# Kernel tuning notes

Measured on AMD Instinct MI355X. Metric: run time of the kernel, lower is better.

## Reference

```python
import jax, jax.numpy as jnp
import numpy as np

N_USER, N_REST, D, E, Q = 200000, 50000, 64, 2000000, 500000


def setup_inputs() -> dict:
    key = jax.random.key(0)
    ks = jax.random.split(key, 16)
    s = 0.05
    return {
        "x_user": jax.random.normal(ks[0], (N_USER, D), jnp.float32),
        "x_rest": jax.random.normal(ks[1], (N_REST, D), jnp.float32),
        "Wl": jax.random.normal(ks[2], (3, 2, D, D), jnp.float32) * s,
        "Wr": jax.random.normal(ks[3], (3, 2, D, D), jnp.float32) * s,
        "bl": jnp.zeros((3, 2, D), jnp.float32),
        "dW1": jax.random.normal(ks[4], (D, 2 * D), jnp.float32) * s,
        "db1": jnp.zeros((D,), jnp.float32),
        "dW2": jax.random.normal(ks[5], (D, D), jnp.float32) * s,
        "db2": jnp.zeros((D,), jnp.float32),
        "dW3": jax.random.normal(ks[6], (1, D), jnp.float32) * s,
        "db3": jnp.zeros((1,), jnp.float32),
        "ur_src": jax.random.randint(ks[7], (E,), 0, N_USER, jnp.int32),
        "ur_dst": jax.random.randint(ks[8], (E,), 0, N_REST, jnp.int32),
        "ru_src": jax.random.randint(ks[9], (E,), 0, N_REST, jnp.int32),
        "ru_dst": jax.random.randint(ks[10], (E,), 0, N_USER, jnp.int32),
        "el_row": jax.random.randint(ks[11], (Q,), 0, N_USER, jnp.int32),
        "el_col": jax.random.randint(ks[12], (Q,), 0, N_REST, jnp.int32),
    }


def _sage(h_src, h_dst, src, dst, W_l, b_l, W_r):
    # PyG SAGEConv: lin_l(mean_{j in N(i)} x_j) + lin_r(x_i); bias on lin_l only.
    n_dst = h_dst.shape[0]
    agg = jax.ops.segment_sum(h_src[src], dst, num_segments=n_dst)  # [n_dst, D]
    cnt = jax.ops.segment_sum(jnp.ones_like(dst, dtype=h_src.dtype), dst, num_segments=n_dst)
    mean = agg / jnp.maximum(cnt, 1)[:, None]
    return mean @ W_l.T + b_l + h_dst @ W_r.T


def reference(x_user, x_rest, Wl, Wr, bl, dW1, db1, dW2, db2, dW3, db3,
              ur_src, ur_dst, ru_src, ru_dst, el_row, el_col):
    hu, hr = x_user, x_rest
    for l in range(3):
        # edge type 0: user -> restaurant ('rates'); edge type 1: reverse
        zr = _sage(hu, hr, ur_src, ur_dst, Wl[l, 0], bl[l, 0], Wr[l, 0])
        zu = _sage(hr, hu, ru_src, ru_dst, Wl[l, 1], bl[l, 1], Wr[l, 1])
        if l < 2:
            zr, zu = jax.nn.relu(zr), jax.nn.relu(zu)
        hu, hr = zu, zr
    # EdgeDecoder
    z = jnp.concatenate([hu[el_row], hr[el_col]], axis=-1)  # [Q, 2D]
    z = jax.nn.relu(z @ dW1.T + db1)
    z = jax.nn.relu(z @ dW2.T + db2)
    z = z @ dW3.T + db3
    return z.reshape(-1)
```

## Files before the change

### kernel.cpp

```cpp
#include <hip/hip_runtime.h>

#define NU 200000
#define NR 50000
#define DD 64
#define NE 2000000
#define NQ 500000
#define NBR 196
#define NBU 782

#define NBS 98
#define BKT_CAP 24576
#define LW_U 11
#define LW_R 9
#define PB_E 4096
#define NPBB 489

__global__ __launch_bounds__(256)
void binpass_kernel(const int* __restrict__ ru_src, const int* __restrict__ ru_dst,
                    const int* __restrict__ ur_src, const int* __restrict__ ur_dst,
                    int* __restrict__ bcur, int2* __restrict__ pairs) {
    __shared__ int2 stg[PB_E];
    __shared__ unsigned char gstg[PB_E];
    __shared__ int hist[256];
    __shared__ int sca[256], scb[256];
    __shared__ int gpos[128];
    int side = (blockIdx.x >= NPBB) ? 1 : 0;
    int blk = side ? (blockIdx.x - NPBB) : blockIdx.x;
    const int* src = side ? ur_src : ru_src;
    const int* dst = side ? ur_dst : ru_dst;
    int lw = side ? LW_R : LW_U;
    int* bc = bcur + side * NBS;
    int2* region = pairs + (size_t)side * NBS * BKT_CAP;
    int tid = threadIdx.x;
    hist[tid] = 0;
    __syncthreads();
    int base = blk * PB_E;
    int myg[16]; int myrank[16]; int2 myp[16];
#pragma unroll
    for (int i = 0; i < 16; i++) {
        int e = base + i * 256 + tid;
        if (e < NE) {
            int d = dst[e];
            int g = d >> lw;
            myg[i] = g;
            myp[i] = make_int2(src[e], d);
            myrank[i] = atomicAdd(&hist[g], 1);
        } else myg[i] = -1;
    }
    __syncthreads();
    int h = hist[tid];
    sca[tid] = h;
    __syncthreads();
    int* cur = sca; int* alt = scb;
    for (int off = 1; off < 256; off <<= 1) {
        int x = cur[tid];
        if (tid >= off) x += cur[tid - off];
        alt[tid] = x;
        __syncthreads();
        int* tmp = cur; cur = alt; alt = tmp;
    }
    alt[tid] = cur[tid] - h;
    if (tid < NBS && h > 0) gpos[tid] = atomicAdd(&bc[tid], h);
    __syncthreads();
    int* basep = alt;
#pragma unroll
    for (int i = 0; i < 16; i++) {
        if (myg[i] >= 0) {
            int p = basep[myg[i]] + myrank[i];
            stg[p] = myp[i];
            gstg[p] = (unsigned char)myg[i];
        }
    }
    __syncthreads();
    int tot = cur[255];
    for (int i = tid; i < tot; i += 256) {
        int g = gstg[i];
        int o = g * BKT_CAP + gpos[g] + (i - basep[g]);
        region[o] = stg[i];
    }
}

__global__ void bbase_kernel(const int* __restrict__ bcur, int* __restrict__ bbase,
                             int* __restrict__ rs_u, int* __restrict__ rs_r) {
    __shared__ int a[128], b[128];
    int sidx = blockIdx.x;
    const int* bc = bcur + sidx * NBS;
    int* bb = bbase + sidx * NBS;
    int tid = threadIdx.x;
    a[tid] = (tid < NBS) ? bc[tid] : 0;
    __syncthreads();
    int* cur = a; int* alt = b;
    for (int off = 1; off < 128; off <<= 1) {
        int t = cur[tid];
        if (tid >= off) t += cur[tid - off];
        alt[tid] = t;
        __syncthreads();
        int* tmp = cur; cur = alt; alt = tmp;
    }
    if (tid < NBS) bb[tid] = (tid == 0) ? 0 : cur[tid - 1];
    if (tid == 0) { if (sidx == 0) rs_u[NU] = NE; else rs_r[NR] = NE; }
}

__global__ __launch_bounds__(256)
void fillpass_kernel(const int2* __restrict__ pairs, const int* __restrict__ bcur,
                     const int* __restrict__ bbase,
                     int* __restrict__ rs_u, int* __restrict__ rs_r,
                     int* __restrict__ csr_u, int* __restrict__ csr_r) {
    __shared__ int win[BKT_CAP];
    __shared__ int lcnt[2048];
    __shared__ int lofs[2048];
    __shared__ int tsc[256], tsc2[256];
    int side = (blockIdx.x >= NBS) ? 1 : 0;
    int bkt = side ? (blockIdx.x - NBS) : blockIdx.x;
    const int2* reg = pairs + ((size_t)side * NBS + bkt) * BKT_CAP;
    int* rs = side ? rs_r : rs_u;
    int* csr = side ? csr_r : csr_u;
    int W = side ? 512 : 2048;
    int lw = side ? LW_R : LW_U;
    int n = side ? NR : NU;
    int d0 = bkt << lw;
    int tot = bcur[side * NBS + bkt];
    int base = bbase[side * NBS + bkt];
    int tid = threadIdx.x;
    for (int i = tid; i < W; i += 256) lcnt[i] = 0;
    __syncthreads();
    for (int i = tid; i < tot; i += 256) {
        int2 p = reg[i];
        atomicAdd(&lcnt[p.y - d0], 1);
    }
    __syncthreads();
    int per = W >> 8;
    int b0 = tid * per;
    int run = 0;
    for (int i = 0; i < per; i++) { int v = lcnt[b0 + i]; lofs[b0 + i] = run; run += v; }
    tsc[tid] = run;
    __syncthreads();
    int* cur = tsc; int* alt = tsc2;
    for (int off = 1; off < 256; off <<= 1) {
        int x = cur[tid];
        if (tid >= off) x += cur[tid - off];
        alt[tid] = x;
        __syncthreads();
        int* tmp = cur; cur = alt; alt = tmp;
    }
    int texcl = cur[tid] - run;
    for (int i = 0; i < per; i++) lofs[b0 + i] += texcl;
    __syncthreads();
    int wn = min(W, n - d0);
    for (int i = tid; i < wn; i += 256) rs[d0 + i] = base + lofs[i];
    __syncthreads();
    for (int i = tid; i < tot; i += 256) {
        int2 p = reg[i];
        int slot = atomicAdd(&lofs[p.y - d0], 1);
        win[slot] = p.x;
    }
    __syncthreads();
    for (int i = tid; i < tot; i += 256) csr[base + i] = win[i];
}

__global__ __launch_bounds__(256)
void gather2_kernel(const float* __restrict__ hu, const int* __restrict__ csr_r,
                    const int* __restrict__ rs_r, float* __restrict__ mean_r,
                    const float* __restrict__ hr, const int* __restrict__ csr_u,
                    const int* __restrict__ rs_u, float* __restrict__ mean_u) {
    int lane = threadIdx.x & 63;
    int wave = blockIdx.x * 4 + (threadIdx.x >> 6);
    const float* h; const int* csr; const int* rs; float* mean; int r;
    if (wave < NR) { h = hu; csr = csr_r; rs = rs_r; mean = mean_r; r = wave; }
    else if (wave < NR + NU) { h = hr; csr = csr_u; rs = rs_u; mean = mean_u; r = wave - NR; }
    else return;
    int s = rs[r], e = rs[r + 1];
    float a0 = 0.f, a1 = 0.f, a2 = 0.f, a3 = 0.f;
    for (int j = s; j < e; j += 64) {
        int rem = e - j;
        int nch = rem < 64 ? rem : 64;
        int li = lane < nch ? lane : nch - 1;
        int idx = csr[j + li];
        for (int kk = 0; kk < nch; kk += 4) {
            int i0 = __shfl(idx, kk);
            int i1 = __shfl(idx, kk + 1);
            int i2 = __shfl(idx, kk + 2);
            int i3 = __shfl(idx, kk + 3);
            float v0 = h[i0 * DD + lane];
            float v1 = h[i1 * DD + lane];
            float v2 = h[i2 * DD + lane];
            float v3 = h[i3 * DD + lane];
            a0 += v0;
            a1 += (kk + 1 < nch) ? v1 : 0.f;
            a2 += (kk + 2 < nch) ? v2 : 0.f;
            a3 += (kk + 3 < nch) ? v3 : 0.f;
        }
    }
    float acc = (a0 + a1) + (a2 + a3);
    float inv = 1.0f / fmaxf((float)(e - s), 1.0f);
    mean[r * DD + lane] = acc * inv;
}

#define DOT4(A, B) ((A).x*(B).x + (A).y*(B).y + (A).z*(B).z + (A).w*(B).w)

#define SDECL(j) float sA##j = bsh[cb + (j)], sB##j = sA##j, sC##j = sA##j, sD##j = sA##j;

#define SCOL(j) { \
    const float4* wlp_ = (const float4*)(Wls + ((cb + (j)) << 6) + kc); \
    const float4* wrp_ = (const float4*)(Wrs + ((cb + (j)) << 6) + kc); \
    float4 l0_ = wlp_[0], l1_ = wlp_[1], q0_ = wrp_[0], q1_ = wrp_[1]; \
    sA##j += DOT4(mA0,l0_)+DOT4(mA1,l1_)+DOT4(xA0,q0_)+DOT4(xA1,q1_); \
    sB##j += DOT4(mB0,l0_)+DOT4(mB1,l1_)+DOT4(xB0,q0_)+DOT4(xB1,q1_); \
    sC##j += DOT4(mC0,l0_)+DOT4(mC1,l1_)+DOT4(xC0,q0_)+DOT4(xC1,q1_); \
    sD##j += DOT4(mD0,l0_)+DOT4(mD1,l1_)+DOT4(xD0,q0_)+DOT4(xD1,q1_); }

#define SRELU(j) { sA##j = fmaxf(sA##j,0.f); sB##j = fmaxf(sB##j,0.f); \
                   sC##j = fmaxf(sC##j,0.f); sD##j = fmaxf(sD##j,0.f); }

#define STORE_ROW(SR, rr) if ((rr) < n) { \
    float* o_ = out + (size_t)(rr) * DD + cb; \
    *(float4*)(o_)      = {SR##0,  SR##1,  SR##2,  SR##3}; \
    *(float4*)(o_ + 4)  = {SR##4,  SR##5,  SR##6,  SR##7}; \
    *(float4*)(o_ + 8)  = {SR##8,  SR##9,  SR##10, SR##11}; \
    *(float4*)(o_ + 12) = {SR##12, SR##13, SR##14, SR##15}; }

__device__ __forceinline__
void sage_tile(const float* __restrict__ mean, const float* __restrict__ h,
               const float* Wls, const float* Wrs, const float* bsh,
               float* __restrict__ out, int n, int do_relu, int r0, int cb) {
    int rA = min(r0, n - 1), rB = min(r0 + 64, n - 1);
    int rC = min(r0 + 128, n - 1), rD = min(r0 + 192, n - 1);
    const float *mA = mean + (size_t)rA * DD, *xA = h + (size_t)rA * DD;
    const float *mB = mean + (size_t)rB * DD, *xB = h + (size_t)rB * DD;
    const float *mC = mean + (size_t)rC * DD, *xC = h + (size_t)rC * DD;
    const float *mD = mean + (size_t)rD * DD, *xD = h + (size_t)rD * DD;
    SDECL(0)  SDECL(1)  SDECL(2)  SDECL(3)  SDECL(4)  SDECL(5)  SDECL(6)  SDECL(7)
    SDECL(8)  SDECL(9)  SDECL(10) SDECL(11) SDECL(12) SDECL(13) SDECL(14) SDECL(15)
#pragma unroll 1
    for (int kc = 0; kc < DD; kc += 8) {
        float4 mA0 = *(const float4*)(mA + kc), mA1 = *(const float4*)(mA + kc + 4);
        float4 xA0 = *(const float4*)(xA + kc), xA1 = *(const float4*)(xA + kc + 4);
        float4 mB0 = *(const float4*)(mB + kc), mB1 = *(const float4*)(mB + kc + 4);
        float4 xB0 = *(const float4*)(xB + kc), xB1 = *(const float4*)(xB + kc + 4);
        float4 mC0 = *(const float4*)(mC + kc), mC1 = *(const float4*)(mC + kc + 4);
        float4 xC0 = *(const float4*)(xC + kc), xC1 = *(const float4*)(xC + kc + 4);
        float4 mD0 = *(const float4*)(mD + kc), mD1 = *(const float4*)(mD + kc + 4);
        float4 xD0 = *(const float4*)(xD + kc), xD1 = *(const float4*)(xD + kc + 4);
        SCOL(0)  SCOL(1)  SCOL(2)  SCOL(3)  SCOL(4)  SCOL(5)  SCOL(6)  SCOL(7)
        SCOL(8)  SCOL(9)  SCOL(10) SCOL(11) SCOL(12) SCOL(13) SCOL(14) SCOL(15)
    }
    if (do_relu) {
        SRELU(0)  SRELU(1)  SRELU(2)  SRELU(3)  SRELU(4)  SRELU(5)  SRELU(6)  SRELU(7)
        SRELU(8)  SRELU(9)  SRELU(10) SRELU(11) SRELU(12) SRELU(13) SRELU(14) SRELU(15)
    }
    STORE_ROW(sA, r0)
    STORE_ROW(sB, r0 + 64)
    STORE_ROW(sC, r0 + 128)
    STORE_ROW(sD, r0 + 192)
}

__global__ __launch_bounds__(256, 2)
void sage_fused_kernel(const float* __restrict__ mean_r, const float* __restrict__ hr,
                       const float* __restrict__ mean_u, const float* __restrict__ hu,
                       const float* __restrict__ Wl2, const float* __restrict__ Wr2,
                       const float* __restrict__ bl2,
                       float* __restrict__ out_r, float* __restrict__ out_u, int do_relu) {
    __shared__ float Wls[DD * DD];
    __shared__ float Wrs[DD * DD];
    __shared__ float bsh[DD];
    int side = (blockIdx.x < NBR) ? 0 : 1;
    const float* Wl = Wl2 + side * DD * DD;
    const float* Wr = Wr2 + side * DD * DD;
    const float* bl = bl2 + side * DD;
    for (int i = threadIdx.x; i < DD * DD; i += 256) {
        Wls[i] = Wl[i];
        Wrs[i] = Wr[i];
    }
    if (threadIdx.x < DD) bsh[threadIdx.x] = bl[threadIdx.x];
    __syncthreads();
    int lane = threadIdx.x & 63;
    int cb = (threadIdx.x >> 6) * 16;
    if (side == 0) {
        int r0 = blockIdx.x * 256 + lane;
        sage_tile(mean_r, hr, Wls, Wrs, bsh, out_r, NR, do_relu, r0, cb);
    } else {
        int r0 = (blockIdx.x - NBR) * 256 + lane;
        sage_tile(mean_u, hu, Wls, Wrs, bsh, out_u, NU, do_relu, r0, cb);
    }
}

#define PCOL(j) { \
    const float4* wp_ = (const float4*)(Ws + ((cb + (j)) << 6) + kc); \
    float4 w0_ = wp_[0], w1_ = wp_[1]; \
    sA##j += DOT4(xA0,w0_)+DOT4(xA1,w1_); \
    sB##j += DOT4(xB0,w0_)+DOT4(xB1,w1_); \
    sC##j += DOT4(xC0,w0_)+DOT4(xC1,w1_); \
    sD##j += DOT4(xD0,w0_)+DOT4(xD1,w1_); }

__device__ __forceinline__
void pre_tile(const float* __restrict__ h, const float* Ws, const float* bsh,
              float* __restrict__ out, int n, int r0, int cb) {
    int rA = min(r0, n - 1), rB = min(r0 + 64, n - 1);
    int rC = min(r0 + 128, n - 1), rD = min(r0 + 192, n - 1);
    const float *xA = h + (size_t)rA * DD, *xB = h + (size_t)rB * DD;
    const float *xC = h + (size_t)rC * DD, *xD = h + (size_t)rD * DD;
    SDECL(0)  SDECL(1)  SDECL(2)  SDECL(3)  SDECL(4)  SDECL(5)  SDECL(6)  SDECL(7)
    SDECL(8)  SDECL(9)  SDECL(10) SDECL(11) SDECL(12) SDECL(13) SDECL(14) SDECL(15)
#pragma unroll 1
    for (int kc = 0; kc < DD; kc += 8) {
        float4 xA0 = *(const float4*)(xA + kc), xA1 = *(const float4*)(xA + kc + 4);
        float4 xB0 = *(const float4*)(xB + kc), xB1 = *(const float4*)(xB + kc + 4);
        float4 xC0 = *(const float4*)(xC + kc), xC1 = *(const float4*)(xC + kc + 4);
        float4 xD0 = *(const float4*)(xD + kc), xD1 = *(const float4*)(xD + kc + 4);
        PCOL(0)  PCOL(1)  PCOL(2)  PCOL(3)  PCOL(4)  PCOL(5)  PCOL(6)  PCOL(7)
        PCOL(8)  PCOL(9)  PCOL(10) PCOL(11) PCOL(12) PCOL(13) PCOL(14) PCOL(15)
    }
    STORE_ROW(sA, r0)
    STORE_ROW(sB, r0 + 64)
    STORE_ROW(sC, r0 + 128)
    STORE_ROW(sD, r0 + 192)
}

__global__ __launch_bounds__(256, 2)
void pre_fused_kernel(const float* __restrict__ hu, const float* __restrict__ hr,
                      const float* __restrict__ dW1, const float* __restrict__ db1,
                      float* __restrict__ P_u, float* __restrict__ P_r) {
    __shared__ float Ws[DD * DD];
    __shared__ float bsh[DD];
    int side = (blockIdx.x < NBU) ? 0 : 1;
    int koff = side ? DD : 0;
    for (int i = threadIdx.x; i < DD * DD; i += 256) {
        int c = i >> 6, k = i & 63;
        Ws[c * DD + k] = dW1[c * 2 * DD + koff + k];
    }
    if (threadIdx.x < DD) bsh[threadIdx.x] = side ? 0.f : db1[threadIdx.x];
    __syncthreads();
    int lane = threadIdx.x & 63;
    int cb = (threadIdx.x >> 6) * 16;
    if (side == 0) {
        int r0 = blockIdx.x * 256 + lane;
        pre_tile(hu, Ws, bsh, P_u, NU, r0, cb);
    } else {
        int r0 = (blockIdx.x - NBU) * 256 + lane;
        pre_tile(hr, Ws, bsh, P_r, NR, r0, cb);
    }
}

#define ZCOMB(Zi, i) float4 Zi; { float4 u_ = pu[i]; float4 v_ = pr[i]; \
    Zi.x = fmaxf(u_.x + v_.x, 0.f); Zi.y = fmaxf(u_.y + v_.y, 0.f); \
    Zi.z = fmaxf(u_.z + v_.z, 0.f); Zi.w = fmaxf(u_.w + v_.w, 0.f); }

__global__ __launch_bounds__(256, 2)
void decoder_kernel(const float* __restrict__ Pu, const float* __restrict__ Pr,
                    const int* __restrict__ el_row, const int* __restrict__ el_col,
                    const float* __restrict__ dW2, const float* __restrict__ db2,
                    const float* __restrict__ dW3, const float* __restrict__ db3,
                    float* __restrict__ out) {
    __shared__ float W2s[DD * DD];
    __shared__ float b2s[DD], w3s[DD];
    for (int i = threadIdx.x; i < DD * DD; i += 256) W2s[i] = dW2[i];
    if (threadIdx.x < DD) {
        b2s[threadIdx.x] = db2[threadIdx.x];
        w3s[threadIdx.x] = dW3[threadIdx.x];
    }
    __syncthreads();
    int q = blockIdx.x * 256 + threadIdx.x;
    if (q >= NQ) return;
    int row = el_row[q], col = el_col[q];
    const float4* pu = (const float4*)(Pu + (size_t)row * DD);
    const float4* pr = (const float4*)(Pr + (size_t)col * DD);
    ZCOMB(z0, 0)  ZCOMB(z1, 1)  ZCOMB(z2, 2)  ZCOMB(z3, 3)
    ZCOMB(z4, 4)  ZCOMB(z5, 5)  ZCOMB(z6, 6)  ZCOMB(z7, 7)
    ZCOMB(z8, 8)  ZCOMB(z9, 9)  ZCOMB(z10, 10) ZCOMB(z11, 11)
    ZCOMB(z12, 12) ZCOMB(z13, 13) ZCOMB(z14, 14) ZCOMB(z15, 15)
    float o = db3[0];
#pragma unroll 2
    for (int c = 0; c < DD; c++) {
        const float4* wp = (const float4*)(W2s + c * DD);
        float s = b2s[c]
            + DOT4(z0, wp[0])  + DOT4(z1, wp[1])  + DOT4(z2, wp[2])  + DOT4(z3, wp[3])
            + DOT4(z4, wp[4])  + DOT4(z5, wp[5])  + DOT4(z6, wp[6])  + DOT4(z7, wp[7])
            + DOT4(z8, wp[8])  + DOT4(z9, wp[9])  + DOT4(z10, wp[10]) + DOT4(z11, wp[11])
            + DOT4(z12, wp[12]) + DOT4(z13, wp[13]) + DOT4(z14, wp[14]) + DOT4(z15, wp[15]);
        o += fmaxf(s, 0.f) * w3s[c];
    }
    out[q] = o;
}

extern "C" void kernel_launch(void* const* d_in, const int* in_sizes, int n_in,
                              void* d_out, int out_size, void* d_ws, size_t ws_size,
                              hipStream_t stream) {
    const float* x_user = (const float*)d_in[0];
    const float* x_rest = (const float*)d_in[1];
    const float* Wl     = (const float*)d_in[2];
    const float* Wr     = (const float*)d_in[3];
    const float* bl     = (const float*)d_in[4];
    const float* dW1    = (const float*)d_in[5];
    const float* db1    = (const float*)d_in[6];
    const float* dW2    = (const float*)d_in[7];
    const float* db2    = (const float*)d_in[8];
    const float* dW3    = (const float*)d_in[9];
    const float* db3    = (const float*)d_in[10];
    const int* ur_src   = (const int*)d_in[11];
    const int* ur_dst   = (const int*)d_in[12];
    const int* ru_src   = (const int*)d_in[13];
    const int* ru_dst   = (const int*)d_in[14];
    const int* el_row   = (const int*)d_in[15];
    const int* el_col   = (const int*)d_in[16];
    float* out = (float*)d_out;

    char* w = (char*)d_ws;
    size_t off = 0;
    auto alloc = [&](size_t bytes) -> void* {
        void* p = (void*)(w + off);
        off += (bytes + 255) & ~(size_t)255;
        return p;
    };
    float* hu0    = (float*)alloc((size_t)NU * DD * 4);
    float* hu1    = (float*)alloc((size_t)NU * DD * 4);
    float* hr0    = (float*)alloc((size_t)NR * DD * 4);
    float* hr1    = (float*)alloc((size_t)NR * DD * 4);
    float* mean_u = (float*)alloc((size_t)NU * DD * 4);
    float* mean_r = (float*)alloc((size_t)NR * DD * 4);
    int* csr_u  = (int*)alloc((size_t)NE * 4);
    int* csr_r  = (int*)alloc((size_t)NE * 4);
    int* rs_u   = (int*)alloc((size_t)(NU + 1) * 4);
    int* rs_r   = (int*)alloc((size_t)(NR + 1) * 4);
    int* bcur   = (int*)alloc((size_t)2 * NBS * 4);
    int* bbase  = (int*)alloc((size_t)2 * NBS * 4);

    int2* pairs = (int2*)mean_u;

    hipMemsetAsync(bcur, 0, (size_t)2 * NBS * 4, stream);
    binpass_kernel<<<2 * NPBB, 256, 0, stream>>>(ru_src, ru_dst, ur_src, ur_dst,
                                                 bcur, pairs);
    bbase_kernel<<<2, 128, 0, stream>>>(bcur, bbase, rs_u, rs_r);
    fillpass_kernel<<<2 * NBS, 256, 0, stream>>>(pairs, bcur, bbase,
                                                 rs_u, rs_r, csr_u, csr_r);

    const float* cu = x_user;
    const float* cr = x_rest;
    float* nu_[3] = {hu0, hu1, hu0};
    float* nr_[3] = {hr0, hr1, hr0};
    const int ggrid = (NR + NU + 3) / 4;

    for (int l = 0; l < 3; l++) {
        const float* Wl2 = Wl + (size_t)l * 2 * DD * DD;
        const float* Wr2 = Wr + (size_t)l * 2 * DD * DD;
        const float* bl2 = bl + (size_t)l * 2 * DD;
        int relu = (l < 2) ? 1 : 0;
        gather2_kernel<<<ggrid, 256, 0, stream>>>(cu, csr_r, rs_r, mean_r,
                                                  cr, csr_u, rs_u, mean_u);
        sage_fused_kernel<<<NBR + NBU, 256, 0, stream>>>(mean_r, cr, mean_u, cu,
                                                         Wl2, Wr2, bl2,
                                                         nr_[l], nu_[l], relu);
        cu = nu_[l];
        cr = nr_[l];
    }
    float* P_u = hu1;
    float* P_r = hr1;
    pre_fused_kernel<<<NBU + NBR, 256, 0, stream>>>(cu, cr, dW1, db1, P_u, P_r);
    decoder_kernel<<<(NQ + 255) / 256, 256, 0, stream>>>(P_u, P_r, el_row, el_col,
                                                         dW2, db2, dW3, db3, out);
}
```

Baseline: 1.180 ms.

## Replace restaurant-side CSR gather with source-sorted LDS scatter accumulation

Restaurant-side aggregation no longer builds a CSR. Instead, edges in each 256-destination bucket are sorted by source id and packed into (src,dst) words. A 512-thread block accumulates hu rows into a 64KB shared-memory tile with LDS atomics, so consecutive blocks read hu in roughly source order for better cache locality, and per-destination counts are computed once. This drops the restaurant CSR fill pass, but only 196 blocks run the scatter step per layer, which uses LDS atomics and gives low occupancy because of the large shared tile.

```diff
diff --git a/kernel.cpp b/kernel.cpp
--- a/kernel.cpp
+++ b/kernel.cpp
@@ -8,12 +8,15 @@
 #define NBR 196
 #define NBU 782
 
-#define NBS 98
-#define BKT_CAP 24576
+#define NBS_U 98
 #define LW_U 11
-#define LW_R 9
+#define CAP_U 24576
+#define NBS_R 196
+#define LW_R 8
+#define CAP_R 12288
 #define PB_E 4096
 #define NPBB 489
+#define SBINS 391
 
 __global__ __launch_bounds__(256)
 void binpass_kernel(const int* __restrict__ ru_src, const int* __restrict__ ru_dst,
@@ -23,14 +26,16 @@
     __shared__ unsigned char gstg[PB_E];
     __shared__ int hist[256];
     __shared__ int sca[256], scb[256];
-    __shared__ int gpos[128];
+    __shared__ int gpos[256];
     int side = (blockIdx.x >= NPBB) ? 1 : 0;
     int blk = side ? (blockIdx.x - NPBB) : blockIdx.x;
     const int* src = side ? ur_src : ru_src;
     const int* dst = side ? ur_dst : ru_dst;
     int lw = side ? LW_R : LW_U;
-    int* bc = bcur + side * NBS;
-    int2* region = pairs + (size_t)side * NBS * BKT_CAP;
+    int nbs = side ? NBS_R : NBS_U;
+    int cap = side ? CAP_R : CAP_U;
+    int* bc = bcur + (side ? NBS_U : 0);
+    int2* region = pairs + (side ? (size_t)NBS_U * CAP_U : 0);
     int tid = threadIdx.x;
     hist[tid] = 0;
     __syncthreads();
@@ -60,7 +65,7 @@
         int* tmp = cur; cur = alt; alt = tmp;
     }
     alt[tid] = cur[tid] - h;
-    if (tid < NBS && h > 0) gpos[tid] = atomicAdd(&bc[tid], h);
+    if (tid < nbs && h > 0) gpos[tid] = atomicAdd(&bc[tid], h);
     __syncthreads();
     int* basep = alt;
 #pragma unroll
@@ -75,19 +80,16 @@
     int tot = cur[255];
     for (int i = tid; i < tot; i += 256) {
         int g = gstg[i];
-        int o = g * BKT_CAP + gpos[g] + (i - basep[g]);
+        int o = g * cap + gpos[g] + (i - basep[g]);
         region[o] = stg[i];
     }
 }
 
-__global__ void bbase_kernel(const int* __restrict__ bcur, int* __restrict__ bbase,
-                             int* __restrict__ rs_u, int* __restrict__ rs_r) {
+__global__ void ubase_kernel(const int* __restrict__ bcur, int* __restrict__ bbase,
+                             int* __restrict__ rs_u) {
     __shared__ int a[128], b[128];
-    int sidx = blockIdx.x;
-    const int* bc = bcur + sidx * NBS;
-    int* bb = bbase + sidx * NBS;
     int tid = threadIdx.x;
-    a[tid] = (tid < NBS) ? bc[tid] : 0;
+    a[tid] = (tid < NBS_U) ? bcur[tid] : 0;
     __syncthreads();
     int* cur = a; int* alt = b;
     for (int off = 1; off < 128; off <<= 1) {
@@ -97,42 +99,34 @@
         __syncthreads();
         int* tmp = cur; cur = alt; alt = tmp;
     }
-    if (tid < NBS) bb[tid] = (tid == 0) ? 0 : cur[tid - 1];
-    if (tid == 0) { if (sidx == 0) rs_u[NU] = NE; else rs_r[NR] = NE; }
+    if (tid < NBS_U) bbase[tid] = (tid == 0) ? 0 : cur[tid - 1];
+    if (tid == 0) rs_u[NU] = NE;
 }
 
 __global__ __launch_bounds__(256)
-void fillpass_kernel(const int2* __restrict__ pairs, const int* __restrict__ bcur,
-                     const int* __restrict__ bbase,
-                     int* __restrict__ rs_u, int* __restrict__ rs_r,
-                     int* __restrict__ csr_u, int* __restrict__ csr_r) {
-    __shared__ int win[BKT_CAP];
+void fillpassu_kernel(const int2* __restrict__ pairs, const int* __restrict__ bcur,
+                      const int* __restrict__ bbase,
+                      int* __restrict__ rs_u, int* __restrict__ csr_u) {
+    __shared__ int win[CAP_U];
     __shared__ int lcnt[2048];
     __shared__ int lofs[2048];
     __shared__ int tsc[256], tsc2[256];
-    int side = (blockIdx.x >= NBS) ? 1 : 0;
-    int bkt = side ? (blockIdx.x - NBS) : blockIdx.x;
-    const int2* reg = pairs + ((size_t)side * NBS + bkt) * BKT_CAP;
-    int* rs = side ? rs_r : rs_u;
-    int* csr = side ? csr_r : csr_u;
-    int W = side ? 512 : 2048;
-    int lw = side ? LW_R : LW_U;
-    int n = side ? NR : NU;
-    int d0 = bkt << lw;
-    int tot = bcur[side * NBS + bkt];
-    int base = bbase[side * NBS + bkt];
+    int bkt = blockIdx.x;
+    const int2* reg = pairs + (size_t)bkt * CAP_U;
+    int d0 = bkt << LW_U;
+    int tot = bcur[bkt];
+    int base = bbase[bkt];
     int tid = threadIdx.x;
-    for (int i = tid; i < W; i += 256) lcnt[i] = 0;
+    for (int i = tid; i < 2048; i += 256) lcnt[i] = 0;
     __syncthreads();
     for (int i = tid; i < tot; i += 256) {
         int2 p = reg[i];
         atomicAdd(&lcnt[p.y - d0], 1);
     }
     __syncthreads();
-    int per = W >> 8;
-    int b0 = tid * per;
+    int b0 = tid * 8;
     int run = 0;
-    for (int i = 0; i < per; i++) { int v = lcnt[b0 + i]; lofs[b0 + i] = run; run += v; }
+    for (int i = 0; i < 8; i++) { int v = lcnt[b0 + i]; lofs[b0 + i] = run; run += v; }
     tsc[tid] = run;
     __syncthreads();
     int* cur = tsc; int* alt = tsc2;
@@ -144,10 +138,10 @@
         int* tmp = cur; cur = alt; alt = tmp;
     }
     int texcl = cur[tid] - run;
-    for (int i = 0; i < per; i++) lofs[b0 + i] += texcl;
-    __syncthreads();
-    int wn = min(W, n - d0);
-    for (int i = tid; i < wn; i += 256) rs[d0 + i] = base + lofs[i];
+    for (int i = 0; i < 8; i++) lofs[b0 + i] += texcl;
+    __syncthreads();
+    int wn = min(2048, NU - d0);
+    for (int i = tid; i < wn; i += 256) rs_u[d0 + i] = base + lofs[i];
     __syncthreads();
     for (int i = tid; i < tot; i += 256) {
         int2 p = reg[i];
@@ -155,36 +149,130 @@
         win[slot] = p.x;
     }
     __syncthreads();
-    for (int i = tid; i < tot; i += 256) csr[base + i] = win[i];
+    for (int i = tid; i < tot; i += 256) csr_u[base + i] = win[i];
 }
 
 __global__ __launch_bounds__(256)
-void gather2_kernel(const float* __restrict__ hu, const int* __restrict__ csr_r,
-                    const int* __restrict__ rs_r, float* __restrict__ mean_r,
-                    const float* __restrict__ hr, const int* __restrict__ csr_u,
+void srcsort_kernel(const int2* __restrict__ pairs, const int* __restrict__ bcur,
+                    int* __restrict__ pairs2, int* __restrict__ cnt_r) {
+    __shared__ int hist[512];
+    __shared__ int cntd[256];
+    __shared__ int tsc[256], tsc2[256];
+    int bkt = blockIdx.x;
+    const int2* reg = pairs + (size_t)NBS_U * CAP_U + (size_t)bkt * CAP_R;
+    int tot = bcur[NBS_U + bkt];
+    int d0 = bkt << LW_R;
+    int tid = threadIdx.x;
+    hist[tid] = 0; hist[tid + 256] = 0; cntd[tid] = 0;
+    __syncthreads();
+    for (int i = tid; i < tot; i += 256) {
+        int2 p = reg[i];
+        atomicAdd(&hist[p.x >> 9], 1);
+        atomicAdd(&cntd[p.y - d0], 1);
+    }
+    __syncthreads();
+    int wn = min(256, NR - d0);
+    if (tid < wn) cnt_r[d0 + tid] = cntd[tid];
+    int b0 = tid * 2;
+    int h0 = hist[b0], h1 = hist[b0 + 1];
+    int run = h0 + h1;
+    tsc[tid] = run;
+    __syncthreads();
+    int* cur = tsc; int* alt = tsc2;
+    for (int off = 1; off < 256; off <<= 1) {
+        int x = cur[tid];
+        if (tid >= off) x += cur[tid - off];
+        alt[tid] = x;
+        __syncthreads();
+        int* tmp = cur; cur = alt; alt = tmp;
+    }
+    int texcl = cur[tid] - run;
+    __syncthreads();
+    hist[b0] = texcl;
+    hist[b0 + 1] = texcl + h0;
+    __syncthreads();
+    for (int i = tid; i < tot; i += 256) {
+        int2 p = reg[i];
+        int pos = atomicAdd(&hist[p.x >> 9], 1);
+        pairs2[(size_t)bkt * CAP_R + pos] = (p.x << LW_R) | (p.y - d0);
+    }
+}
+
+__global__ __launch_bounds__(512, 1)
+void rscatter_kernel(const float* __restrict__ hu, const int* __restrict__ pairs2,
+                     const int* __restrict__ bcur, const int* __restrict__ cnt_r,
+                     float* __restrict__ mean_r) {
+    __shared__ float acc[256 * DD];
+    int bkt = blockIdx.x;
+    int tot = bcur[NBS_U + bkt];
+    int d0 = bkt << LW_R;
+    const int* reg = pairs2 + (size_t)bkt * CAP_R;
+    int tid = threadIdx.x;
+    for (int i = tid; i < 256 * DD; i += 512) acc[i] = 0.f;
+    __syncthreads();
+    int lane = tid & 63;
+    int wv = tid >> 6;
+    for (int c = wv * 64; c < tot; c += 512) {
+        int n = min(64, tot - c);
+        int v = reg[c + (lane < n ? lane : n - 1)];
+        for (int k = 0; k < n; k += 8) {
+            int v0 = __shfl(v, k);
+            int v1 = __shfl(v, k + 1);
+            int v2 = __shfl(v, k + 2);
+            int v3 = __shfl(v, k + 3);
+            int v4 = __shfl(v, k + 4);
+            int v5 = __shfl(v, k + 5);
+            int v6 = __shfl(v, k + 6);
+            int v7 = __shfl(v, k + 7);
+            float x0 = hu[(size_t)(v0 >> LW_R) * DD + lane];
+            float x1 = hu[(size_t)(v1 >> LW_R) * DD + lane];
+            float x2 = hu[(size_t)(v2 >> LW_R) * DD + lane];
+            float x3 = hu[(size_t)(v3 >> LW_R) * DD + lane];
+            float x4 = hu[(size_t)(v4 >> LW_R) * DD + lane];
+            float x5 = hu[(size_t)(v5 >> LW_R) * DD + lane];
+            float x6 = hu[(size_t)(v6 >> LW_R) * DD + lane];
+            float x7 = hu[(size_t)(v7 >> LW_R) * DD + lane];
+            atomicAdd(&acc[(v0 & 255) * DD + lane], x0);
+            if (k + 1 < n) atomicAdd(&acc[(v1 & 255) * DD + lane], x1);
+            if (k + 2 < n) atomicAdd(&acc[(v2 & 255) * DD + lane], x2);
+            if (k + 3 < n) atomicAdd(&acc[(v3 & 255) * DD + lane], x3);
+            if (k + 4 < n) atomicAdd(&acc[(v4 & 255) * DD + lane], x4);
+            if (k + 5 < n) atomicAdd(&acc[(v5 & 255) * DD + lane], x5);
+            if (k + 6 < n) atomicAdd(&acc[(v6 & 255) * DD + lane], x6);
+            if (k + 7 < n) atomicAdd(&acc[(v7 & 255) * DD + lane], x7);
+        }
+    }
+    __syncthreads();
+    int wn = min(256, NR - d0);
+    for (int rr = wv; rr < wn; rr += 8) {
+        float inv = 1.0f / fmaxf((float)cnt_r[d0 + rr], 1.0f);
+        mean_r[(size_t)(d0 + rr) * DD + lane] = acc[rr * DD + lane] * inv;
+    }
+}
+
+__global__ __launch_bounds__(256)
+void gatheru_kernel(const float* __restrict__ hr, const int* __restrict__ csr_u,
                     const int* __restrict__ rs_u, float* __restrict__ mean_u) {
     int lane = threadIdx.x & 63;
     int wave = blockIdx.x * 4 + (threadIdx.x >> 6);
-    const float* h; const int* csr; const int* rs; float* mean; int r;
-    if (wave < NR) { h = hu; csr = csr_r; rs = rs_r; mean = mean_r; r = wave; }
-    else if (wave < NR + NU) { h = hr; csr = csr_u; rs = rs_u; mean = mean_u; r = wave - NR; }
-    else return;
-    int s = rs[r], e = rs[r + 1];
+    if (wave >= NU) return;
+    int r = wave;
+    int s = rs_u[r], e = rs_u[r + 1];
     float a0 = 0.f, a1 = 0.f, a2 = 0.f, a3 = 0.f;
     for (int j = s; j < e; j += 64) {
         int rem = e - j;
         int nch = rem < 64 ? rem : 64;
         int li = lane < nch ? lane : nch - 1;
-        int idx = csr[j + li];
+        int idx = csr_u[j + li];
         for (int kk = 0; kk < nch; kk += 4) {
             int i0 = __shfl(idx, kk);
             int i1 = __shfl(idx, kk + 1);
             int i2 = __shfl(idx, kk + 2);
             int i3 = __shfl(idx, kk + 3);
-            float v0 = h[i0 * DD + lane];
-            float v1 = h[i1 * DD + lane];
-            float v2 = h[i2 * DD + lane];
-            float v3 = h[i3 * DD + lane];
+            float v0 = hr[i0 * DD + lane];
+            float v1 = hr[i1 * DD + lane];
+            float v2 = hr[i2 * DD + lane];
+            float v3 = hr[i3 * DD + lane];
             a0 += v0;
             a1 += (kk + 1 < nch) ? v1 : 0.f;
             a2 += (kk + 2 < nch) ? v2 : 0.f;
@@ -193,7 +281,7 @@
     }
     float acc = (a0 + a1) + (a2 + a3);
     float inv = 1.0f / fmaxf((float)(e - s), 1.0f);
-    mean[r * DD + lane] = acc * inv;
+    mean_u[r * DD + lane] = acc * inv;
 }
 
 #define DOT4(A, B) ((A).x*(B).x + (A).y*(B).y + (A).z*(B).z + (A).w*(B).w)
@@ -418,34 +506,34 @@
     float* mean_u = (float*)alloc((size_t)NU * DD * 4);
     float* mean_r = (float*)alloc((size_t)NR * DD * 4);
     int* csr_u  = (int*)alloc((size_t)NE * 4);
-    int* csr_r  = (int*)alloc((size_t)NE * 4);
     int* rs_u   = (int*)alloc((size_t)(NU + 1) * 4);
-    int* rs_r   = (int*)alloc((size_t)(NR + 1) * 4);
-    int* bcur   = (int*)alloc((size_t)2 * NBS * 4);
-    int* bbase  = (int*)alloc((size_t)2 * NBS * 4);
+    int* cnt_r  = (int*)alloc((size_t)NR * 4);
+    int* pairs2 = (int*)alloc((size_t)NBS_R * CAP_R * 4);
+    int* bcur   = (int*)alloc((size_t)(NBS_U + NBS_R) * 4);
+    int* bbase  = (int*)alloc((size_t)NBS_U * 4);
 
     int2* pairs = (int2*)mean_u;
 
-    hipMemsetAsync(bcur, 0, (size_t)2 * NBS * 4, stream);
+    hipMemsetAsync(bcur, 0, (size_t)(NBS_U + NBS_R) * 4, stream);
     binpass_kernel<<<2 * NPBB, 256, 0, stream>>>(ru_src, ru_dst, ur_src, ur_dst,
                                                  bcur, pairs);
-    bbase_kernel<<<2, 128, 0, stream>>>(bcur, bbase, rs_u, rs_r);
-    fillpass_kernel<<<2 * NBS, 256, 0, stream>>>(pairs, bcur, bbase,
-                                                 rs_u, rs_r, csr_u, csr_r);
+    ubase_kernel<<<1, 128, 0, stream>>>(bcur, bbase, rs_u);
+    fillpassu_kernel<<<NBS_U, 256, 0, stream>>>(pairs, bcur, bbase, rs_u, csr_u);
+    srcsort_kernel<<<NBS_R, 256, 0, stream>>>(pairs, bcur, pairs2, cnt_r);
 
     const float* cu = x_user;
     const float* cr = x_rest;
     float* nu_[3] = {hu0, hu1, hu0};
     float* nr_[3] = {hr0, hr1, hr0};
-    const int ggrid = (NR + NU + 3) / 4;
+    const int ugrid = (NU + 3) / 4;
 
     for (int l = 0; l < 3; l++) {
         const float* Wl2 = Wl + (size_t)l * 2 * DD * DD;
         const float* Wr2 = Wr + (size_t)l * 2 * DD * DD;
         const float* bl2 = bl + (size_t)l * 2 * DD;
         int relu = (l < 2) ? 1 : 0;
-        gather2_kernel<<<ggrid, 256, 0, stream>>>(cu, csr_r, rs_r, mean_r,
-                                                  cr, csr_u, rs_u, mean_u);
+        rscatter_kernel<<<NBS_R, 512, 0, stream>>>(cu, pairs2, bcur, cnt_r, mean_r);
+        gatheru_kernel<<<ugrid, 256, 0, stream>>>(cr, csr_u, rs_u, mean_u);
         sage_fused_kernel<<<NBR + NBU, 256, 0, stream>>>(mean_r, cr, mean_u, cu,
                                                          Wl2, Wr2, bl2,
                                                          nr_[l], nu_[l], relu);
```

Result: slower. 3.732 ms (+216.3%).
